# Kernel optimization log

Measured on AMD Instinct MI355X. Metric: run time of the kernel, lower is better.

## Reference

```python
import jax, jax.numpy as jnp
import numpy as np
import hashlib

# Model hyperparameters (from VictorASIFractalLightModel defaults)
B, L, D = 2, 2048, 1024
VOCAB, TOOL_VOCAB = 65536, 128
STEPS = 8            # FractalEmbedding steps -> 2*STEPS = 16 features
N_CONV, N_ATTN = 10, 6
HEADS, Q_GROUPS = 8, 2
HPG = HEADS // Q_GROUPS
HEAD_DIM = D // HEADS
KSIZE = 5
EPS = 1e-5


def _token_to_c(token_ids_np):
    # sha256-based complex constant per token id (exactly as in FractalEmbedding)
    flat = token_ids_np.reshape(-1)
    out = np.empty((flat.size, 2), dtype=np.float32)
    for i, tid in enumerate(flat):
        h = hashlib.sha256(str(int(tid)).encode()).hexdigest()
        out[i, 0] = (int(h[:16], 16) / 2**64 - 0.5) * 2.0
        out[i, 1] = (int(h[16:32], 16) / 2**64 - 0.5) * 2.0
    return out.reshape(token_ids_np.shape + (2,))


def _julia_feats(cs):
    # Vectorized julia iteration, z starts at 0.  cs: [B, L, 2] -> feats [B, L, 2*STEPS]
    cr, ci = cs[..., 0], cs[..., 1]
    zr = jnp.zeros_like(cr)
    zi = jnp.zeros_like(ci)
    feats = []
    for _ in range(STEPS):
        zr, zi = zr * zr - zi * zi + cr, 2.0 * zr * zi + ci
        feats.append(zr)
        feats.append(zi)
    return jnp.stack(feats, axis=-1)


def _layer_norm(x, s, b):
    mu = jnp.mean(x, axis=-1, keepdims=True)
    var = jnp.mean(jnp.square(x - mu), axis=-1, keepdims=True)
    return (x - mu) * jax.lax.rsqrt(var + EPS) * s + b


def _conv_block(x, dw_w, dw_b, pw_w, pw_b, ln_s, ln_b):
    # x: [B, L, D] -> depthwise conv (k=5, same pad) -> pointwise conv to 2D -> GLU -> residual LN
    xc = jnp.transpose(x, (0, 2, 1))  # [B, D, L]
    y = jax.lax.conv_general_dilated(xc, dw_w, (1,), [(KSIZE // 2, KSIZE // 2)],
                                     dimension_numbers=("NCH", "OIH", "NCH"),
                                     feature_group_count=D) + dw_b[None, :, None]
    y = jax.lax.conv_general_dilated(y, pw_w, (1,), [(0, 0)],
                                     dimension_numbers=("NCH", "OIH", "NCH")) + pw_b[None, :, None]
    y = jnp.transpose(y, (0, 2, 1))  # [B, L, 2D]
    a, gate = jnp.split(y, 2, axis=-1)
    return _layer_norm(x + a * jax.nn.sigmoid(gate), ln_s, ln_b)


def _attention(x, qw, kvw, ow, ln_s, ln_b):
    # Grouped-query attention with an explicit (unfused) score tensor, per the source.
    Bx, Lx, Dx = x.shape
    q = (x @ qw).reshape(Bx, Lx, Q_GROUPS, HPG, HEAD_DIM)
    kv = (x @ kvw).reshape(Bx, Lx, HEADS, 2, HEAD_DIM)
    k = kv[..., 0, :].reshape(Bx, Lx, Q_GROUPS, HPG, HEAD_DIM)
    v = kv[..., 1, :].reshape(Bx, Lx, Q_GROUPS, HPG, HEAD_DIM)
    scale = HEAD_DIM ** -0.5
    scores = jnp.einsum("bqghd,bkghd->bghqk", q, k) * scale  # [B, g, hpg, Lq, Lk]
    attn = jax.nn.softmax(scores, axis=-1)
    out = jnp.einsum("bghqk,bkghd->bqghd", attn, v).reshape(Bx, Lx, Dx)
    return _layer_norm(x + out @ ow, ln_s, ln_b)


def setup_inputs() -> dict:
    key = jax.random.key(0)
    ks = jax.random.split(key, 10)
    token_ids = jax.random.randint(ks[0], (B, L), 0, VOCAB)
    cs = jnp.asarray(_token_to_c(np.asarray(token_ids)))
    return {
        "token_ids": token_ids,
        "cs": cs,
        "proj_w": jax.random.normal(ks[1], (2 * STEPS, D), dtype=jnp.float32) * 0.25,
        "emb_scale": jnp.ones((1,), dtype=jnp.float32),
        "conv_dw_w": jax.random.normal(ks[2], (N_CONV, D, 1, KSIZE), dtype=jnp.float32) * 0.2,
        "conv_dw_b": jnp.zeros((N_CONV, D), dtype=jnp.float32),
        "conv_pw_w": jax.random.normal(ks[3], (N_CONV, 2 * D, D, 1), dtype=jnp.float32) * (D ** -0.5),
        "conv_pw_b": jnp.zeros((N_CONV, 2 * D), dtype=jnp.float32),
        "conv_ln_s": jnp.ones((N_CONV, D), dtype=jnp.float32),
        "conv_ln_b": jnp.zeros((N_CONV, D), dtype=jnp.float32),
        "attn_q_w": jax.random.normal(ks[4], (N_ATTN, D, D), dtype=jnp.float32) * (D ** -0.5),
        "attn_kv_w": jax.random.normal(ks[5], (N_ATTN, D, 2 * D), dtype=jnp.float32) * (D ** -0.5),
        "attn_out_w": jax.random.normal(ks[6], (N_ATTN, D, D), dtype=jnp.float32) * (D ** -0.5),
        "attn_ln_s": jnp.ones((N_ATTN, D), dtype=jnp.float32),
        "attn_ln_b": jnp.zeros((N_ATTN, D), dtype=jnp.float32),
        "lm_w": jax.random.normal(ks[7], (D, VOCAB), dtype=jnp.float32) * (D ** -0.5),
        "tool_w": jax.random.normal(ks[8], (D, TOOL_VOCAB), dtype=jnp.float32) * (D ** -0.5),
        "tool_b": jnp.zeros((TOOL_VOCAB,), dtype=jnp.float32),
    }


def reference(token_ids, cs, proj_w, emb_scale, conv_dw_w, conv_dw_b, conv_pw_w, conv_pw_b,
              conv_ln_s, conv_ln_b, attn_q_w, attn_kv_w, attn_out_w, attn_ln_s, attn_ln_b,
              lm_w, tool_w, tool_b):
    feats = _julia_feats(cs)                 # [B, L, 16]
    h = (feats @ proj_w) * emb_scale         # FractalEmbedding
    for i in range(N_CONV):
        h = _conv_block(h, conv_dw_w[i], conv_dw_b[i], conv_pw_w[i], conv_pw_b[i],
                        conv_ln_s[i], conv_ln_b[i])
    for i in range(N_ATTN):
        h = _attention(h, attn_q_w[i], attn_kv_w[i], attn_out_w[i], attn_ln_s[i], attn_ln_b[i])
    # ReplayMemoryStack is a side-effecting identity on h.
    last = h[:, -1, :]
    gen_logits = last @ lm_w
    tool_logits = last @ tool_w + tool_b
    return gen_logits, tool_logits
```

## Files before the change

### kernel.cpp

```cpp
#include <hip/hip_runtime.h>
#include <hip/hip_bf16.h>
#include <math.h>

#define B_ 2
#define L_ 2048
#define D_ 1024
#define VOCAB_ 65536
#define TOOLV_ 128
#define NCONV_ 10
#define NATTN_ 6
#define HEADS_ 8
#define HD_ 128
#define EPS_ 1e-5f

typedef short bf16x8 __attribute__((ext_vector_type(8)));
typedef short short4v __attribute__((ext_vector_type(4)));
typedef float f32x4 __attribute__((ext_vector_type(4)));
#define MFMA16(a,b,c) __builtin_amdgcn_mfma_f32_16x16x32_bf16(a, b, c, 0, 0, 0)

__device__ inline short f2bf(float f) {
  __hip_bfloat16 h = __float2bfloat16(f);
  return *reinterpret_cast<short*>(&h);
}

__device__ __forceinline__ void gld16(const void* g, void* l) {
  __builtin_amdgcn_global_load_lds(
      (const __attribute__((address_space(1))) unsigned int*)g,
      (__attribute__((address_space(3))) unsigned int*)l, 16, 0, 0);
}

__device__ __forceinline__ void sync_prefetch() {
  asm volatile("s_waitcnt vmcnt(0)" ::: "memory");
  __builtin_amdgcn_s_barrier();
  __builtin_amdgcn_sched_barrier(0);
}

__global__ __launch_bounds__(256) void julia_proj_k(const float* __restrict__ cs,
    const float* __restrict__ pw, const float* __restrict__ esc, float* __restrict__ h) {
  int row = blockIdx.x;
  float cr = cs[2*(size_t)row], ci = cs[2*(size_t)row+1];
  float f[16];
  float zr = 0.f, zi = 0.f;
  #pragma unroll
  for (int s = 0; s < 8; ++s) {
    float nzr = zr*zr - zi*zi + cr;
    float nzi = 2.f*zr*zi + ci;
    zr = nzr; zi = nzi;
    f[2*s] = zr; f[2*s+1] = zi;
  }
  float e = esc[0];
  int d = threadIdx.x * 4;
  float4 acc = {0.f, 0.f, 0.f, 0.f};
  #pragma unroll
  for (int i = 0; i < 16; ++i) {
    float4 pv = *(const float4*)(pw + i*D_ + d);
    acc.x += f[i]*pv.x; acc.y += f[i]*pv.y; acc.z += f[i]*pv.z; acc.w += f[i]*pv.w;
  }
  acc.x *= e; acc.y *= e; acc.z *= e; acc.w *= e;
  *(float4*)(h + (size_t)row*D_ + d) = acc;
}

__global__ __launch_bounds__(256) void dwconv_k(const float* __restrict__ x,
    const float* __restrict__ w, const float* __restrict__ bias, short* __restrict__ y) {
  int idx = blockIdx.x*256 + threadIdx.x;
  int d = (idx & (D_/4 - 1)) * 4;
  int bl = idx >> 8;
  int l = bl & (L_-1);
  size_t bbase = (size_t)(bl >> 11) * L_;
  float4 acc = *(const float4*)(bias + d);
  float wr[4][5];
  #pragma unroll
  for (int j = 0; j < 4; ++j)
    #pragma unroll
    for (int k = 0; k < 5; ++k) wr[j][k] = w[(d+j)*5 + k];
  #pragma unroll
  for (int k = 0; k < 5; ++k) {
    int ll = l + k - 2;
    if (ll >= 0 && ll < L_) {
      float4 xv = *(const float4*)(x + (bbase + ll)*D_ + d);
      acc.x += xv.x*wr[0][k]; acc.y += xv.y*wr[1][k];
      acc.z += xv.z*wr[2][k]; acc.w += xv.w*wr[3][k];
    }
  }
  short4v o = { f2bf(acc.x), f2bf(acc.y), f2bf(acc.z), f2bf(acc.w) };
  ((short4v*)y)[idx] = o;
}

__global__ __launch_bounds__(256) void cvt_perm_k(const float* __restrict__ W,
    short* __restrict__ out) {
  int z = blockIdx.y;
  int i4 = blockIdx.x*256 + threadIdx.x;
  int e = i4*4;
  int r = e >> 10, k = e & 1023;
  int t = r >> 7, wn = (r >> 6) & 1, j = r & 63;
  int u = t*64 + wn*32 + (j & 31);
  int src = (j < 32) ? u : 1024 + u;
  const float* p = W + ((size_t)z*2048 + src)*1024 + k;
  float4 v = *(const float4*)p;
  short4v s = { f2bf(v.x), f2bf(v.y), f2bf(v.z), f2bf(v.w) };
  *(short4v*)(out + ((size_t)z*2048 + r)*1024 + k) = s;
}

__global__ __launch_bounds__(256) void transp_bf16_k(const float* __restrict__ W0,
    short* __restrict__ WT0, int K, int N, size_t srcStride, size_t dstStride) {
  const float* W = W0 + blockIdx.z*srcStride;
  short* WT = WT0 + blockIdx.z*dstStride;
  __shared__ short t[32][33];
  int n0 = blockIdx.x*32, k0 = blockIdx.y*32;
  int tx = threadIdx.x & 31, ty = threadIdx.x >> 5;
  #pragma unroll
  for (int i = 0; i < 4; ++i) {
    int k = ty + i*8;
    t[tx][k] = f2bf(W[(size_t)(k0+k)*N + n0 + tx]);
  }
  __syncthreads();
  #pragma unroll
  for (int i = 0; i < 4; ++i) {
    int n = ty + i*8;
    WT[(size_t)(n0+n)*K + k0 + tx] = t[n][tx];
  }
}

template<int MODE, int BN>
__global__ __launch_bounds__(256) void gemm_bf16(const short* __restrict__ A,
    const short* __restrict__ Bt, const float* __restrict__ bias,
    float* __restrict__ C, short* __restrict__ obf,
    short* __restrict__ kbf, short* __restrict__ vtbf,
    float scale, int M, int N, int K) {
  constexpr int NI = BN/32;
  __shared__ short As[2][128*32];
  __shared__ short Bs[2][BN*32];
  const int tid  = threadIdx.x;
  const int lane = tid & 63;
  const int wave = tid >> 6;
  const int wm = wave >> 1, wn = wave & 1;
  const int g = lane >> 4, c = lane & 15;

  int flat = blockIdx.y * gridDim.x + blockIdx.x;
  int nwg  = gridDim.x * gridDim.y;
  int swz  = (flat & 7) * (nwg >> 3) + (flat >> 3);
  const int m0 = (swz & 31) * 128;
  const int n0 = (swz >> 5) * BN;

  f32x4 acc[4][NI];
  #pragma unroll
  for (int i = 0; i < 4; ++i)
    #pragma unroll
    for (int j = 0; j < NI; ++j) acc[i][j] = (f32x4){0.f,0.f,0.f,0.f};

  const int srow = wave*16 + (lane>>2);
  const int scol = (lane&3)*8;
  const short* aSrc0 = A + (size_t)(m0 + srow)*K + scol;
  const short* aSrc1 = aSrc0 + (size_t)64*K;
  const short* bSrc0 = Bt + (size_t)(n0 + srow)*K + scol;
  const short* bSrc1 = bSrc0 + (size_t)64*K;
  const int woff = wave*512;

  gld16(aSrc0, &As[0][woff]);
  gld16(aSrc1, &As[0][woff + 2048]);
  gld16(bSrc0, &Bs[0][woff]);
  if (BN == 128) gld16(bSrc1, &Bs[0][woff + 2048]);
  sync_prefetch();

  const int nt = K >> 5;
  int cur = 0;
  for (int t = 0; t < nt; ++t) {
    if (t + 1 < nt) {
      int k0 = (t + 1) << 5;
      gld16(aSrc0 + k0, &As[cur^1][woff]);
      gld16(aSrc1 + k0, &As[cur^1][woff + 2048]);
      gld16(bSrc0 + k0, &Bs[cur^1][woff]);
      if (BN == 128) gld16(bSrc1 + k0, &Bs[cur^1][woff + 2048]);
    }
    bf16x8 af[4], bfr[NI];
    #pragma unroll
    for (int mi = 0; mi < 4; ++mi)
      af[mi] = *(const bf16x8*)&As[cur][(wm*64 + mi*16 + c)*32 + g*8];
    #pragma unroll
    for (int ni = 0; ni < NI; ++ni)
      bfr[ni] = *(const bf16x8*)&Bs[cur][(wn*(BN/2) + ni*16 + c)*32 + g*8];
    #pragma unroll
    for (int mi = 0; mi < 4; ++mi)
      #pragma unroll
      for (int ni = 0; ni < NI; ++ni)
        acc[mi][ni] = MFMA16(af[mi], bfr[ni], acc[mi][ni]);
    if (t + 1 < nt) {
      sync_prefetch();
      cur ^= 1;
    }
  }

  if (MODE == 4) {
    #pragma unroll
    for (int mi = 0; mi < 4; ++mi) {
      int row = m0 + wm*64 + mi*16 + g*4;
      #pragma unroll
      for (int ni = 0; ni < 2; ++ni) {
        int u = (n0 >> 7)*64 + wn*32 + ni*16 + c;
        float ba = bias[u], bg = bias[1024 + u];
        #pragma unroll
        for (int r = 0; r < 4; ++r) {
          float a  = acc[mi][ni][r]   + ba;
          float gt = acc[mi][ni+2][r] + bg;
          C[(size_t)(row+r)*1024 + u] = a / (1.f + expf(-gt));
        }
      }
    }
    return;
  }

  #pragma unroll
  for (int mi = 0; mi < 4; ++mi) {
    int row = m0 + wm*64 + mi*16 + g*4;
    #pragma unroll
    for (int ni = 0; ni < NI; ++ni) {
      int col = n0 + wn*(BN/2) + ni*16 + c;
      if (MODE == 0) {
        #pragma unroll
        for (int r = 0; r < 4; ++r)
          C[(size_t)(row+r)*N + col] = acc[mi][ni][r];
      } else {
        if (col < 1024) {
          #pragma unroll
          for (int r = 0; r < 4; ++r)
            obf[(size_t)(row+r)*1024 + col] = f2bf(acc[mi][ni][r]*scale);
        } else {
          int col2 = col - 1024;
          int hh = col2 >> 8, jj = (col2 >> 7) & 1, d = col2 & 127;
          int bb = row >> 11, l = row & 2047;
          size_t bh = (size_t)bb*8 + hh;
          if (jj == 0) {
            #pragma unroll
            for (int r = 0; r < 4; ++r)
              kbf[(bh*L_ + l + r)*128 + d] = f2bf(acc[mi][ni][r]);
          } else {
            #pragma unroll
            for (int r = 0; r < 4; ++r)
              vtbf[(bh*128 + d)*L_ + l + r] = f2bf(acc[mi][ni][r]);
          }
        }
      }
    }
  }
}

__global__ __launch_bounds__(256) void resid_ln_k(float* __restrict__ h,
    const float* __restrict__ proj, const float* __restrict__ s, const float* __restrict__ b,
    short* __restrict__ bo) {
  int row = blockIdx.x;
  int tid = threadIdx.x;
  int d = tid*4;
  float* xr = h + (size_t)row*D_;
  const float* pr = proj + (size_t)row*D_;
  __shared__ float red[256];
  float4 xv = *(const float4*)(xr + d);
  float4 pv = *(const float4*)(pr + d);
  float v[4] = { xv.x+pv.x, xv.y+pv.y, xv.z+pv.z, xv.w+pv.w };
  red[tid] = v[0]+v[1]+v[2]+v[3]; __syncthreads();
  for (int st = 128; st > 0; st >>= 1) { if (tid < st) red[tid] += red[tid+st]; __syncthreads(); }
  float mu = red[0] * (1.f/D_); __syncthreads();
  float lv = 0.f;
  #pragma unroll
  for (int j = 0; j < 4; ++j) { float dd = v[j]-mu; lv += dd*dd; }
  red[tid] = lv; __syncthreads();
  for (int st = 128; st > 0; st >>= 1) { if (tid < st) red[tid] += red[tid+st]; __syncthreads(); }
  float var = red[0] * (1.f/D_);
  float r = 1.f/sqrtf(var + EPS_);
  float4 sv = *(const float4*)(s + d);
  float4 bv = *(const float4*)(b + d);
  float4 o;
  o.x = (v[0]-mu)*r*sv.x + bv.x;
  o.y = (v[1]-mu)*r*sv.y + bv.y;
  o.z = (v[2]-mu)*r*sv.z + bv.z;
  o.w = (v[3]-mu)*r*sv.w + bv.w;
  *(float4*)(xr + d) = o;
  if (bo) {
    short4v ob = { f2bf(o.x), f2bf(o.y), f2bf(o.z), f2bf(o.w) };
    *(short4v*)(bo + (size_t)row*D_ + d) = ob;
  }
}

#define PPITCH 72
__global__ __launch_bounds__(256) void attn2_k(const short* __restrict__ qbf,
    const short* __restrict__ kbf, const short* __restrict__ vtbf,
    short* __restrict__ obf) {
  __shared__ short Ks[2][64*128];
  __shared__ short Vts[2][128*64];
  __shared__ short Ps[4*16*PPITCH];

  const int tid  = threadIdx.x;
  const int wave = tid >> 6;
  const int lane = tid & 63;
  const int g    = lane >> 4;
  const int c    = lane & 15;

  int flat = blockIdx.x;
  int swz  = (flat & 7)*64 + (flat >> 3);
  const int qt = swz & 31;
  const int hh = (swz >> 5) & 7;
  const int b  = swz >> 8;
  const int q0 = qt*64 + wave*16;
  const size_t bh = (size_t)(b*HEADS_ + hh);

  bf16x8 qf[4];
  {
    const short* Qp = qbf + ((size_t)(b*L_ + q0 + c))*D_ + hh*HD_;
    #pragma unroll
    for (int kd = 0; kd < 4; ++kd)
      qf[kd] = *(const bf16x8*)(Qp + kd*32 + g*8);
  }

  f32x4 O[8];
  #pragma unroll
  for (int i = 0; i < 8; ++i) O[i] = (f32x4){0.f,0.f,0.f,0.f};
  float mrun[4] = {-INFINITY,-INFINITY,-INFINITY,-INFINITY};
  float lrun[4] = {0.f,0.f,0.f,0.f};
  short* Pw = Ps + wave*16*PPITCH;

  const short* kBase = kbf + bh*L_*128;
  const short* vBase = vtbf + bh*128*L_;

  auto stage = [&](int t, int buf) {
    #pragma unroll
    for (int rd = 0; rd < 4; ++rd) {
      int slot = rd*256 + tid;
      int kr = slot >> 4, kj = slot & 15;
      int vr = slot >> 3, vj = slot & 7;
      gld16(kBase + ((size_t)(t*64 + kr))*128 + ((kj ^ (kr & 15)) * 8),
            (char*)&Ks[buf][0] + (rd*256 + wave*64)*16);
      gld16(vBase + (size_t)vr*L_ + t*64 + ((vj ^ (vr & 7)) * 8),
            (char*)&Vts[buf][0] + (rd*256 + wave*64)*16);
    }
  };

  stage(0, 0);
  sync_prefetch();
  int cur = 0;
  const int NT = L_/64;

  for (int t = 0; t < NT; ++t) {
    if (t + 1 < NT) stage(t + 1, cur^1);

    f32x4 s[4];
    #pragma unroll
    for (int nc = 0; nc < 4; ++nc) {
      s[nc] = (f32x4){0.f,0.f,0.f,0.f};
      int R = nc*16 + c;
      #pragma unroll
      for (int kd = 0; kd < 4; ++kd) {
        bf16x8 kf = *(const bf16x8*)&Ks[cur][R*128 + (((kd*4 + g) ^ (R & 15)) * 8)];
        s[nc] = MFMA16(qf[kd], kf, s[nc]);
      }
    }

    float tm[4], rsum[4], alpha[4];
    #pragma unroll
    for (int r = 0; r < 4; ++r)
      tm[r] = fmaxf(fmaxf(s[0][r], s[1][r]), fmaxf(s[2][r], s[3][r]));
    #pragma unroll
    for (int r = 0; r < 4; ++r) {
      #pragma unroll
      for (int mask = 1; mask <= 8; mask <<= 1)
        tm[r] = fmaxf(tm[r], __shfl_xor(tm[r], mask));
      float mnew = fmaxf(mrun[r], tm[r]);
      alpha[r] = expf(mrun[r] - mnew);
      mrun[r] = mnew;
      rsum[r] = 0.f;
    }
    #pragma unroll
    for (int nc = 0; nc < 4; ++nc)
      #pragma unroll
      for (int r = 0; r < 4; ++r) {
        float p = expf(s[nc][r] - mrun[r]);
        s[nc][r] = p;
        rsum[r] += p;
      }
    #pragma unroll
    for (int r = 0; r < 4; ++r) {
      #pragma unroll
      for (int mask = 1; mask <= 8; mask <<= 1)
        rsum[r] += __shfl_xor(rsum[r], mask);
      lrun[r] = lrun[r]*alpha[r] + rsum[r];
    }
    #pragma unroll
    for (int nc = 0; nc < 8; ++nc)
      #pragma unroll
      for (int r = 0; r < 4; ++r) O[nc][r] *= alpha[r];

    #pragma unroll
    for (int nc = 0; nc < 4; ++nc)
      #pragma unroll
      for (int r = 0; r < 4; ++r)
        Pw[(g*4+r)*PPITCH + nc*16 + c] = f2bf(s[nc][r]);
    asm volatile("s_waitcnt lgkmcnt(0)" ::: "memory");
    bf16x8 pa0 = *(const bf16x8*)&Pw[c*PPITCH + g*8];
    bf16x8 pa1 = *(const bf16x8*)&Pw[c*PPITCH + 32 + g*8];

    #pragma unroll
    for (int ks = 0; ks < 2; ++ks) {
      #pragma unroll
      for (int nc = 0; nc < 8; ++nc) {
        int R = nc*16 + c;
        bf16x8 vf = *(const bf16x8*)&Vts[cur][R*64 + (((ks*4 + g) ^ (R & 7)) * 8)];
        O[nc] = MFMA16(ks ? pa1 : pa0, vf, O[nc]);
      }
    }

    if (t + 1 < NT) {
      sync_prefetch();
      cur ^= 1;
    }
  }

  short* ob = obf + ((size_t)(b*L_ + q0))*D_ + hh*HD_;
  #pragma unroll
  for (int r = 0; r < 4; ++r) {
    float inv = 1.f / lrun[r];
    #pragma unroll
    for (int nc = 0; nc < 8; ++nc)
      ob[(size_t)(g*4+r)*D_ + nc*16 + c] = f2bf(O[nc][r] * inv);
  }
}

__global__ __launch_bounds__(256) void lm_head_part_k(const float* __restrict__ h,
    const float* __restrict__ lm_w, float* __restrict__ part) {
  int tid = threadIdx.x;
  int n = (blockIdx.x*256 + tid)*4;
  int ks = blockIdx.y;
  __shared__ float last0[128], last1[128];
  const float* h0 = h + ((size_t)0*L_ + (L_-1))*D_ + ks*128;
  const float* h1 = h + ((size_t)1*L_ + (L_-1))*D_ + ks*128;
  if (tid < 128) { last0[tid] = h0[tid]; last1[tid] = h1[tid]; }
  __syncthreads();
  float4 a0 = {0.f,0.f,0.f,0.f}, a1 = {0.f,0.f,0.f,0.f};
  const float* wp = lm_w + (size_t)(ks*128)*VOCAB_ + n;
  for (int kk = 0; kk < 128; ++kk) {
    float4 wv = *(const float4*)(wp + (size_t)kk*VOCAB_);
    float c0 = last0[kk], c1 = last1[kk];
    a0.x += c0*wv.x; a0.y += c0*wv.y; a0.z += c0*wv.z; a0.w += c0*wv.w;
    a1.x += c1*wv.x; a1.y += c1*wv.y; a1.z += c1*wv.z; a1.w += c1*wv.w;
  }
  *(float4*)(part + ((size_t)ks*2 + 0)*VOCAB_ + n) = a0;
  *(float4*)(part + ((size_t)ks*2 + 1)*VOCAB_ + n) = a1;
}

__global__ __launch_bounds__(256) void lm_head_red_k(const float* __restrict__ part,
    float* __restrict__ out) {
  int i = blockIdx.x*256 + threadIdx.x;
  int j = (i*4) / VOCAB_;
  int n = (i*4) & (VOCAB_-1);
  float4 acc = {0.f,0.f,0.f,0.f};
  #pragma unroll
  for (int ks = 0; ks < 8; ++ks) {
    float4 v = *(const float4*)(part + ((size_t)ks*2 + j)*VOCAB_ + n);
    acc.x += v.x; acc.y += v.y; acc.z += v.z; acc.w += v.w;
  }
  *(float4*)(out + (size_t)j*VOCAB_ + n) = acc;
}

__global__ __launch_bounds__(128) void tool_head_k(const float* __restrict__ h,
    const float* __restrict__ tw, const float* __restrict__ tb, float* __restrict__ out) {
  int b = blockIdx.x;
  int tid = threadIdx.x;
  __shared__ float last[D_];
  const float* hr = h + ((size_t)b*L_ + (L_-1))*D_;
  for (int d = tid; d < D_; d += 128) last[d] = hr[d];
  __syncthreads();
  float acc = tb[tid];
  for (int k = 0; k < D_; ++k) acc += last[k]*tw[(size_t)k*TOOLV_ + tid];
  out[(size_t)2*VOCAB_ + (size_t)b*TOOLV_ + tid] = acc;
}

extern "C" void kernel_launch(void* const* d_in, const int* in_sizes, int n_in,
                              void* d_out, int out_size, void* d_ws, size_t ws_size,
                              hipStream_t stream) {
  const float* cs        = (const float*)d_in[1];
  const float* proj_w    = (const float*)d_in[2];
  const float* emb_scale = (const float*)d_in[3];
  const float* conv_dw_w = (const float*)d_in[4];
  const float* conv_dw_b = (const float*)d_in[5];
  const float* conv_pw_w = (const float*)d_in[6];
  const float* conv_pw_b = (const float*)d_in[7];
  const float* conv_ln_s = (const float*)d_in[8];
  const float* conv_ln_b = (const float*)d_in[9];
  const float* attn_q_w  = (const float*)d_in[10];
  const float* attn_kv_w = (const float*)d_in[11];
  const float* attn_out_w= (const float*)d_in[12];
  const float* attn_ln_s = (const float*)d_in[13];
  const float* attn_ln_b = (const float*)d_in[14];
  const float* lm_w      = (const float*)d_in[15];
  const float* tool_w    = (const float*)d_in[16];
  const float* tool_b    = (const float*)d_in[17];

  const int M = B_*L_;
  float* h    = (float*)d_ws;
  float* buf2 = h    + (size_t)M*D_;
  short* kbf  = (short*)(buf2 + (size_t)M*2*D_);
  short* vtbf = kbf + (size_t)B_*HEADS_*L_*128;
  short* abf  = (short*)(vtbf + (size_t)B_*HEADS_*128*L_);
  short* wconv= abf + (size_t)M*D_;
  short* wqkv = wconv + (size_t)NCONV_*2*D_*D_;
  short* wout = wqkv + (size_t)NATTN_*3*D_*D_;
  float* lmpart = (float*)(wout + (size_t)NATTN_*D_*D_);
  short* qbf  = (short*)(buf2 + (size_t)M*D_);

  const float scale = 0.088388347648318447f;

  {
    cvt_perm_k<<<dim3((2*D_*D_/4)/256, NCONV_), 256, 0, stream>>>(conv_pw_w, wconv);
    transp_bf16_k<<<dim3(D_/32, D_/32, NATTN_), 256, 0, stream>>>(
        attn_q_w, wqkv, D_, D_, (size_t)D_*D_, (size_t)3*D_*D_);
    transp_bf16_k<<<dim3((2*D_)/32, D_/32, NATTN_), 256, 0, stream>>>(
        attn_kv_w, wqkv + (size_t)D_*D_, D_, 2*D_, (size_t)D_*2*D_, (size_t)3*D_*D_);
    transp_bf16_k<<<dim3(D_/32, D_/32, NATTN_), 256, 0, stream>>>(
        attn_out_w, wout, D_, D_, (size_t)D_*D_, (size_t)D_*D_);
  }

  julia_proj_k<<<M, 256, 0, stream>>>(cs, proj_w, emb_scale, h);

  for (int i = 0; i < NCONV_; ++i) {
    dwconv_k<<<(M*D_/4)/256, 256, 0, stream>>>(h, conv_dw_w + (size_t)i*D_*5,
                                               conv_dw_b + (size_t)i*D_, abf);
    gemm_bf16<4, 128><<<dim3(M/128, (2*D_)/128), 256, 0, stream>>>(
        abf, wconv + (size_t)i*2*D_*D_, conv_pw_b + (size_t)i*2*D_,
        buf2, nullptr, nullptr, nullptr, 1.f, M, 2*D_, D_);
    resid_ln_k<<<M, 256, 0, stream>>>(h, buf2, conv_ln_s + (size_t)i*D_,
                                      conv_ln_b + (size_t)i*D_,
                                      (i == NCONV_-1) ? abf : (short*)nullptr);
  }

  for (int i = 0; i < NATTN_; ++i) {
    gemm_bf16<3, 128><<<dim3(M/128, (3*D_)/128), 256, 0, stream>>>(
        abf, wqkv + (size_t)i*3*D_*D_, nullptr, nullptr, qbf, kbf, vtbf,
        scale, M, 3*D_, D_);
    attn2_k<<<(L_/64)*HEADS_*B_, 256, 0, stream>>>(qbf, kbf, vtbf, abf);
    gemm_bf16<0, 64><<<dim3(M/128, D_/64), 256, 0, stream>>>(
        abf, wout + (size_t)i*D_*D_, nullptr, buf2, nullptr, nullptr, nullptr,
        1.f, M, D_, D_);
    resid_ln_k<<<M, 256, 0, stream>>>(h, buf2, attn_ln_s + (size_t)i*D_,
                                      attn_ln_b + (size_t)i*D_,
                                      (i < NATTN_-1) ? abf : (short*)nullptr);
  }

  lm_head_part_k<<<dim3(VOCAB_/1024, 8), 256, 0, stream>>>(h, lm_w, lmpart);
  lm_head_red_k<<<(2*VOCAB_/4)/256, 256, 0, stream>>>(lmpart, (float*)d_out);
  tool_head_k<<<B_, 128, 0, stream>>>(h, tool_w, tool_b, (float*)d_out);
}
```

Measured before the change: 1.804 ms.

## Fuse residual LayerNorm with next layer's depthwise conv using halo rows

A new kernel applies the residual add and LayerNorm for one conv block, then immediately computes the next block's depthwise conv from a shared-memory tile. Each 8-row tile recomputes LayerNorm for 2 halo rows on each side. The hidden state now ping-pongs between two buffers, which avoids a race between neighbouring blocks. This removes a separate dwconv launch and its re-read of h per layer, at the cost of about 1.5x LayerNorm reads and extra workspace. It also merges the q and out weight transposes into one launch.

```diff
diff --git a/kernel.cpp b/kernel.cpp
--- a/kernel.cpp
+++ b/kernel.cpp
@@ -84,6 +84,99 @@
   }
   short4v o = { f2bf(acc.x), f2bf(acc.y), f2bf(acc.z), f2bf(acc.w) };
   ((short4v*)y)[idx] = o;
+}
+
+__global__ __launch_bounds__(256) void ln_dwconv_k(const float* __restrict__ hIn,
+    const float* __restrict__ glu, const float* __restrict__ lns,
+    const float* __restrict__ lnb, const float* __restrict__ dww,
+    const float* __restrict__ dwb, float* __restrict__ hOut,
+    short* __restrict__ abf) {
+  __shared__ float lds[12][1028];
+  const int tid = threadIdx.x;
+  const int wv = tid >> 6, ln = tid & 63;
+  const int r0 = blockIdx.x * 8;
+  const int bb = r0 >> 11;
+
+  float4 sv[4], bv[4];
+  #pragma unroll
+  for (int q = 0; q < 4; ++q) {
+    int d = ln*4 + q*256;
+    sv[q] = *(const float4*)(lns + d);
+    bv[q] = *(const float4*)(lnb + d);
+  }
+
+  #pragma unroll
+  for (int i = 0; i < 3; ++i) {
+    int lr = wv*3 + i;
+    int gl = r0 - 2 + lr;
+    bool valid = (gl >= (bb << 11)) && (gl < ((bb + 1) << 11));
+    if (valid) {
+      float4 v4[4];
+      float ssum = 0.f;
+      #pragma unroll
+      for (int q = 0; q < 4; ++q) {
+        int d = ln*4 + q*256;
+        float4 xv = *(const float4*)(hIn + (size_t)gl*D_ + d);
+        float4 pv = *(const float4*)(glu + (size_t)gl*D_ + d);
+        v4[q].x = xv.x+pv.x; v4[q].y = xv.y+pv.y;
+        v4[q].z = xv.z+pv.z; v4[q].w = xv.w+pv.w;
+        ssum += v4[q].x + v4[q].y + v4[q].z + v4[q].w;
+      }
+      #pragma unroll
+      for (int mask = 1; mask < 64; mask <<= 1) ssum += __shfl_xor(ssum, mask);
+      float mu = ssum * (1.f/D_);
+      float vs = 0.f;
+      #pragma unroll
+      for (int q = 0; q < 4; ++q) {
+        float dx = v4[q].x-mu, dy = v4[q].y-mu, dz = v4[q].z-mu, dw = v4[q].w-mu;
+        vs += dx*dx + dy*dy + dz*dz + dw*dw;
+      }
+      #pragma unroll
+      for (int mask = 1; mask < 64; mask <<= 1) vs += __shfl_xor(vs, mask);
+      float rr = 1.f/sqrtf(vs*(1.f/D_) + EPS_);
+      #pragma unroll
+      for (int q = 0; q < 4; ++q) {
+        int d = ln*4 + q*256;
+        float4 o4;
+        o4.x = (v4[q].x-mu)*rr*sv[q].x + bv[q].x;
+        o4.y = (v4[q].y-mu)*rr*sv[q].y + bv[q].y;
+        o4.z = (v4[q].z-mu)*rr*sv[q].z + bv[q].z;
+        o4.w = (v4[q].w-mu)*rr*sv[q].w + bv[q].w;
+        *(float4*)&lds[lr][d] = o4;
+        if (lr >= 2 && lr < 10)
+          *(float4*)(hOut + (size_t)gl*D_ + d) = o4;
+      }
+    } else {
+      float4 z = {0.f,0.f,0.f,0.f};
+      #pragma unroll
+      for (int q = 0; q < 4; ++q)
+        *(float4*)&lds[lr][ln*4 + q*256] = z;
+    }
+  }
+  __syncthreads();
+
+  int o = tid >> 5;
+  int cb = (tid & 31) * 4;
+  int grow = r0 + o;
+  #pragma unroll
+  for (int p = 0; p < 8; ++p) {
+    int d = cb + p*128;
+    float wf[20];
+    #pragma unroll
+    for (int j = 0; j < 5; ++j)
+      *(float4*)&wf[j*4] = *(const float4*)(dww + d*5 + j*4);
+    float4 acc = *(const float4*)(dwb + d);
+    #pragma unroll
+    for (int k = 0; k < 5; ++k) {
+      float4 lv = *(const float4*)&lds[o + k][d];
+      acc.x += lv.x * wf[k];
+      acc.y += lv.y * wf[5 + k];
+      acc.z += lv.z * wf[10 + k];
+      acc.w += lv.w * wf[15 + k];
+    }
+    short4v ov = { f2bf(acc.x), f2bf(acc.y), f2bf(acc.z), f2bf(acc.w) };
+    *(short4v*)(abf + (size_t)grow*D_ + d) = ov;
+  }
 }
 
 __global__ __launch_bounds__(256) void cvt_perm_k(const float* __restrict__ W,
@@ -118,6 +211,29 @@
   for (int i = 0; i < 4; ++i) {
     int n = ty + i*8;
     WT[(size_t)(n0+n)*K + k0 + tx] = t[n][tx];
+  }
+}
+
+__global__ __launch_bounds__(256) void transp_qo_k(const float* __restrict__ Wq,
+    const float* __restrict__ Wo, short* __restrict__ WTq, short* __restrict__ WTo) {
+  int z = blockIdx.z;
+  const float* W;
+  short* WT;
+  if (z < NATTN_) { W = Wq + (size_t)z*D_*D_; WT = WTq + (size_t)z*3*D_*D_; }
+  else { W = Wo + (size_t)(z-NATTN_)*D_*D_; WT = WTo + (size_t)(z-NATTN_)*D_*D_; }
+  __shared__ short t[32][33];
+  int n0 = blockIdx.x*32, k0 = blockIdx.y*32;
+  int tx = threadIdx.x & 31, ty = threadIdx.x >> 5;
+  #pragma unroll
+  for (int i = 0; i < 4; ++i) {
+    int k = ty + i*8;
+    t[tx][k] = f2bf(W[(size_t)(k0+k)*D_ + n0 + tx]);
+  }
+  __syncthreads();
+  #pragma unroll
+  for (int i = 0; i < 4; ++i) {
+    int n = ty + i*8;
+    WT[(size_t)(n0+n)*D_ + k0 + tx] = t[n][tx];
   }
 }
 
@@ -493,8 +609,9 @@
   const float* tool_b    = (const float*)d_in[17];
 
   const int M = B_*L_;
-  float* h    = (float*)d_ws;
-  float* buf2 = h    + (size_t)M*D_;
+  float* hA   = (float*)d_ws;
+  float* hB   = hA   + (size_t)M*D_;
+  float* buf2 = hB   + (size_t)M*D_;
   short* kbf  = (short*)(buf2 + (size_t)M*2*D_);
   short* vtbf = kbf + (size_t)B_*HEADS_*L_*128;
   short* abf  = (short*)(vtbf + (size_t)B_*HEADS_*128*L_);
@@ -508,26 +625,33 @@
 
   {
     cvt_perm_k<<<dim3((2*D_*D_/4)/256, NCONV_), 256, 0, stream>>>(conv_pw_w, wconv);
-    transp_bf16_k<<<dim3(D_/32, D_/32, NATTN_), 256, 0, stream>>>(
-        attn_q_w, wqkv, D_, D_, (size_t)D_*D_, (size_t)3*D_*D_);
+    transp_qo_k<<<dim3(D_/32, D_/32, 2*NATTN_), 256, 0, stream>>>(
+        attn_q_w, attn_out_w, wqkv, wout);
     transp_bf16_k<<<dim3((2*D_)/32, D_/32, NATTN_), 256, 0, stream>>>(
         attn_kv_w, wqkv + (size_t)D_*D_, D_, 2*D_, (size_t)D_*2*D_, (size_t)3*D_*D_);
-    transp_bf16_k<<<dim3(D_/32, D_/32, NATTN_), 256, 0, stream>>>(
-        attn_out_w, wout, D_, D_, (size_t)D_*D_, (size_t)D_*D_);
-  }
-
-  julia_proj_k<<<M, 256, 0, stream>>>(cs, proj_w, emb_scale, h);
-
-  for (int i = 0; i < NCONV_; ++i) {
-    dwconv_k<<<(M*D_/4)/256, 256, 0, stream>>>(h, conv_dw_w + (size_t)i*D_*5,
-                                               conv_dw_b + (size_t)i*D_, abf);
+  }
+
+  julia_proj_k<<<M, 256, 0, stream>>>(cs, proj_w, emb_scale, hA);
+
+  dwconv_k<<<(M*D_/4)/256, 256, 0, stream>>>(hA, conv_dw_w, conv_dw_b, abf);
+
+  float* hc = hA;
+  float* hn = hB;
+  for (int i = 0; i < NCONV_ - 1; ++i) {
     gemm_bf16<4, 128><<<dim3(M/128, (2*D_)/128), 256, 0, stream>>>(
         abf, wconv + (size_t)i*2*D_*D_, conv_pw_b + (size_t)i*2*D_,
         buf2, nullptr, nullptr, nullptr, 1.f, M, 2*D_, D_);
-    resid_ln_k<<<M, 256, 0, stream>>>(h, buf2, conv_ln_s + (size_t)i*D_,
-                                      conv_ln_b + (size_t)i*D_,
-                                      (i == NCONV_-1) ? abf : (short*)nullptr);
-  }
+    ln_dwconv_k<<<M/8, 256, 0, stream>>>(hc, buf2,
+        conv_ln_s + (size_t)i*D_, conv_ln_b + (size_t)i*D_,
+        conv_dw_w + (size_t)(i+1)*D_*5, conv_dw_b + (size_t)(i+1)*D_,
+        hn, abf);
+    float* tmp = hc; hc = hn; hn = tmp;
+  }
+  gemm_bf16<4, 128><<<dim3(M/128, (2*D_)/128), 256, 0, stream>>>(
+      abf, wconv + (size_t)(NCONV_-1)*2*D_*D_, conv_pw_b + (size_t)(NCONV_-1)*2*D_,
+      buf2, nullptr, nullptr, nullptr, 1.f, M, 2*D_, D_);
+  resid_ln_k<<<M, 256, 0, stream>>>(hc, buf2,
+      conv_ln_s + (size_t)(NCONV_-1)*D_, conv_ln_b + (size_t)(NCONV_-1)*D_, abf);
 
   for (int i = 0; i < NATTN_; ++i) {
     gemm_bf16<3, 128><<<dim3(M/128, (3*D_)/128), 256, 0, stream>>>(
@@ -537,12 +661,12 @@
     gemm_bf16<0, 64><<<dim3(M/128, D_/64), 256, 0, stream>>>(
         abf, wout + (size_t)i*D_*D_, nullptr, buf2, nullptr, nullptr, nullptr,
         1.f, M, D_, D_);
-    resid_ln_k<<<M, 256, 0, stream>>>(h, buf2, attn_ln_s + (size_t)i*D_,
+    resid_ln_k<<<M, 256, 0, stream>>>(hc, buf2, attn_ln_s + (size_t)i*D_,
                                       attn_ln_b + (size_t)i*D_,
                                       (i < NATTN_-1) ? abf : (short*)nullptr);
   }
 
-  lm_head_part_k<<<dim3(VOCAB_/1024, 8), 256, 0, stream>>>(h, lm_w, lmpart);
+  lm_head_part_k<<<dim3(VOCAB_/1024, 8), 256, 0, stream>>>(hc, lm_w, lmpart);
   lm_head_red_k<<<(2*VOCAB_/4)/256, 256, 0, stream>>>(lmpart, (float*)d_out);
-  tool_head_k<<<B_, 128, 0, stream>>>(h, tool_w, tool_b, (float*)d_out);
-}
+  tool_head_k<<<B_, 128, 0, stream>>>(hc, tool_w, tool_b, (float*)d_out);
+}
```

Measured after the change: 1.692 ms. 6.2% less time.
